# Performance work log

Measured on AMD Instinct MI355X. Metric: run time of the kernel, lower is better.

The kernel has to match this reference:

```python
import jax, jax.numpy as jnp
import numpy as np

EMB = 512
HID = 1024
BATCH = 64
TX = 512


def setup_inputs() -> dict:
    key = jax.random.key(0)
    ks = jax.random.split(key, 9)
    s = 0.05
    return {
        "word": jax.random.normal(ks[0], (BATCH, TX, EMB), dtype=jnp.float32),
        "Wz": jax.random.normal(ks[1], (HID, HID + EMB), dtype=jnp.float32) * s,
        "bz": jax.random.normal(ks[2], (HID,), dtype=jnp.float32) * s,
        "Wr": jax.random.normal(ks[3], (HID, HID + EMB), dtype=jnp.float32) * s,
        "br": jax.random.normal(ks[4], (HID,), dtype=jnp.float32) * s,
        "Wh": jax.random.normal(ks[5], (HID, HID + EMB), dtype=jnp.float32) * s,
        "bh": jax.random.normal(ks[6], (HID,), dtype=jnp.float32) * s,
        "Wy": jax.random.normal(ks[7], (EMB, HID), dtype=jnp.float32) * s,
        "by": jax.random.normal(ks[8], (EMB,), dtype=jnp.float32) * s,
    }


def reference(word, Wz, bz, Wr, br, Wh, bh, Wy, by):
    batch = word.shape[0]
    word_t = jnp.transpose(word, (1, 0, 2))  # [T, B, E]
    h0 = jnp.zeros((batch, HID), dtype=word.dtype)
    x0 = jnp.zeros((batch, EMB), dtype=word.dtype)

    def step(carry, w_i):
        h, x = carry  # x is the PREVIOUS timestep's word (lags by one, as in the torch code)
        comb = jnp.concatenate([h, x], axis=1)  # [B, HID+EMB]
        z = jax.nn.sigmoid(comb @ Wz.T + bz)
        r = jax.nn.sigmoid(comb @ Wr.T + br)
        comb2 = jnp.concatenate([r * h, x], axis=1)
        h_tilde = jnp.tanh(comb2 @ Wh.T + bh)
        h_new = (1.0 - z) * h + z * h_tilde
        y = h_new @ Wy.T + by  # [B, E]
        return (h_new, w_i), y

    _, ys = jax.lax.scan(step, (h0, x0), word_t)  # ys: [T, B, E]
    return jnp.transpose(ys, (1, 0, 2))  # [B, T, E]
```

## Files before the change

### kernel.cpp

```cpp
#include <hip/hip_runtime.h>
#include <hip/hip_bf16.h>


#define EMB 512
#define HID 1024
#define BATCHN 64
#define TLEN 512
#define CAT 1536
#define GROUPS 4
#define GB 16
#define WPG 32
#define HX_LD 1024
#define ZL_LD 34
#define GPAD 8

typedef __attribute__((ext_vector_type(8))) short bf16x8;
typedef __attribute__((ext_vector_type(4))) short s16x4;
typedef __attribute__((ext_vector_type(4))) float f32x4;
typedef unsigned int u32;
typedef unsigned long long u64;
typedef unsigned short u16;

__device__ __forceinline__ float bf2f(u16 u) {
  union { float f; u32 i; } v; v.i = ((u32)u) << 16; return v.f;
}
__device__ __forceinline__ u16 f2bf(float f) {
  union { float f; u32 i; } v; v.f = f;
  u32 r = v.i + 0x7fffu + ((v.i >> 16) & 1u);
  return (u16)(r >> 16);
}

__device__ __forceinline__ u64 ld_dc(const u16* p) {
  return __hip_atomic_load((const u64*)p, __ATOMIC_RELAXED, __HIP_MEMORY_SCOPE_AGENT);
}
__device__ __forceinline__ void st_dc16(u16* p, u16 v) {
  __hip_atomic_store(p, v, __ATOMIC_RELAXED, __HIP_MEMORY_SCOPE_AGENT);
}

__global__ __launch_bounds__(256) void convert_gate_w(const float* __restrict__ W,
                                                      u16* __restrict__ Wh_,
                                                      u16* __restrict__ Wx_) {
  int i = blockIdx.x * 256 + threadIdx.x;
  if (i >= HID * CAT) return;
  int row = i / CAT, col = i - row * CAT;
  u16 v = f2bf(W[i]);
  if (col < HID) Wh_[row * HID + col] = v;
  else           Wx_[row * EMB + (col - HID)] = v;
}

__global__ __launch_bounds__(256) void convert_wy(const float* __restrict__ W, u16* __restrict__ Wy_) {
  int i = blockIdx.x * 256 + threadIdx.x;
  if (i < EMB * HID) Wy_[i] = f2bf(W[i]);
}

__global__ __launch_bounds__(256) void proj3_kernel(
    const float* __restrict__ word,
    const u16* __restrict__ Wzx, const u16* __restrict__ Wrx, const u16* __restrict__ Whx,
    const float* __restrict__ bz, const float* __restrict__ br, const float* __restrict__ bh,
    u16* __restrict__ Pz, u16* __restrict__ Pr, u16* __restrict__ Ph) {
  __shared__ __align__(16) u16 As[128][64 + GPAD];
  __shared__ __align__(16) u16 Bs[3][64][64 + GPAD];
  const int tid = threadIdx.x;
  const int wid = tid >> 6, lane = tid & 63;
  const int m0 = blockIdx.x * 128, n0 = blockIdx.y * 64;
  const int mw = wid * 32;
  const u16* __restrict__ Wx[3] = {Wzx, Wrx, Whx};
  f32x4 acc[3][2][4] = {};
  for (int k0 = 0; k0 < EMB; k0 += 64) {
#pragma unroll
    for (int it = 0; it < 8; ++it) {
      int e = (it * 256 + tid) * 4;
      int row = e >> 6, col = e & 63;
      int R = m0 + row;
      float4 a = make_float4(0.f, 0.f, 0.f, 0.f);
      if ((R & (TLEN - 1)) != 0)
        a = *reinterpret_cast<const float4*>(&word[(u64)(R - 1) * EMB + k0 + col]);
      s16x4 vv;
      vv[0] = (short)f2bf(a.x); vv[1] = (short)f2bf(a.y);
      vv[2] = (short)f2bf(a.z); vv[3] = (short)f2bf(a.w);
      *reinterpret_cast<s16x4*>(&As[row][col]) = vv;
    }
#pragma unroll
    for (int p = 0; p < 3; ++p)
#pragma unroll
      for (int it = 0; it < 2; ++it) {
        int e = (it * 256 + tid) * 8;
        int row = e >> 6, col = e & 63;
        *reinterpret_cast<bf16x8*>(&Bs[p][row][col]) =
            *reinterpret_cast<const bf16x8*>(&Wx[p][(u64)(n0 + row) * EMB + k0 + col]);
      }
    __syncthreads();
#pragma unroll
    for (int kk = 0; kk < 2; ++kk) {
      const int kb = kk * 32 + 8 * (lane >> 4);
#pragma unroll
      for (int i = 0; i < 2; ++i) {
        bf16x8 a = *reinterpret_cast<const bf16x8*>(&As[mw + i * 16 + (lane & 15)][kb]);
#pragma unroll
        for (int p = 0; p < 3; ++p)
#pragma unroll
          for (int j = 0; j < 4; ++j) {
            bf16x8 b = *reinterpret_cast<const bf16x8*>(&Bs[p][j * 16 + (lane & 15)][kb]);
            acc[p][i][j] = __builtin_amdgcn_mfma_f32_16x16x32_bf16(a, b, acc[p][i][j], 0, 0, 0);
          }
      }
    }
    __syncthreads();
  }
  u16* __restrict__ Pout[3] = {Pz, Pr, Ph};
  const float* __restrict__ bias[3] = {bz, br, bh};
#pragma unroll
  for (int p = 0; p < 3; ++p)
#pragma unroll
    for (int i = 0; i < 2; ++i)
#pragma unroll
      for (int j = 0; j < 4; ++j) {
        int col = n0 + j * 16 + (lane & 15);
        float bv = bias[p][col];
#pragma unroll
        for (int q = 0; q < 4; ++q) {
          int row = m0 + mw + i * 16 + 4 * (lane >> 4) + q;
          Pout[p][(u64)row * HID + col] = f2bf(acc[p][i][j][q] + bv);
        }
      }
}

__global__ __launch_bounds__(256) void out_gemm(const u16* __restrict__ H,
                                                const u16* __restrict__ Wy,
                                                const float* __restrict__ by,
                                                float* __restrict__ out) {
  __shared__ __align__(16) u16 As[128][64 + GPAD];
  __shared__ __align__(16) u16 Bs[64][64 + GPAD];
  const int tid = threadIdx.x;
  const int wid = tid >> 6, lane = tid & 63;
  const int m0 = blockIdx.x * 128, n0 = blockIdx.y * 64;
  const int mw = wid * 32;
  f32x4 acc[2][4] = {};
  for (int k0 = 0; k0 < HID; k0 += 64) {
#pragma unroll
    for (int it = 0; it < 4; ++it) {
      int e = (it * 256 + tid) * 8;
      int row = e >> 6, col = e & 63;
      *reinterpret_cast<bf16x8*>(&As[row][col]) =
          *reinterpret_cast<const bf16x8*>(&H[(u64)(m0 + row) * HID + k0 + col]);
    }
#pragma unroll
    for (int it = 0; it < 2; ++it) {
      int e = (it * 256 + tid) * 8;
      int row = e >> 6, col = e & 63;
      *reinterpret_cast<bf16x8*>(&Bs[row][col]) =
          *reinterpret_cast<const bf16x8*>(&Wy[(u64)(n0 + row) * HID + k0 + col]);
    }
    __syncthreads();
#pragma unroll
    for (int kk = 0; kk < 2; ++kk) {
      const int kb = kk * 32 + 8 * (lane >> 4);
#pragma unroll
      for (int i = 0; i < 2; ++i) {
        bf16x8 a = *reinterpret_cast<const bf16x8*>(&As[mw + i * 16 + (lane & 15)][kb]);
#pragma unroll
        for (int j = 0; j < 4; ++j) {
          bf16x8 b = *reinterpret_cast<const bf16x8*>(&Bs[j * 16 + (lane & 15)][kb]);
          acc[i][j] = __builtin_amdgcn_mfma_f32_16x16x32_bf16(a, b, acc[i][j], 0, 0, 0);
        }
      }
    }
    __syncthreads();
  }
#pragma unroll
  for (int i = 0; i < 2; ++i)
#pragma unroll
    for (int j = 0; j < 4; ++j) {
      int col = n0 + j * 16 + (lane & 15);
      float bv = by[col];
#pragma unroll
      for (int q = 0; q < 4; ++q) {
        int row = m0 + mw + i * 16 + 4 * (lane >> 4) + q;
        out[(u64)row * EMB + col] = acc[i][j][q] + bv;
      }
    }
}

__device__ __forceinline__ void poll_flags_wave(u32* gflags, u32 target) {
  const int lane = threadIdx.x & 63;
  const int active = (lane < WPG) ? 1 : 0;
  u32* addr = &gflags[(lane & (WPG - 1)) * 16];
  for (;;) {
    u32 v = target;
    if (active)
      v = __hip_atomic_load(addr, __ATOMIC_RELAXED, __HIP_MEMORY_SCOPE_AGENT);
    if (!__any((int)(v < target))) break;
  }
}

__global__ __launch_bounds__(256, 1) void gru_persistent(
    const u16* __restrict__ Wzh, const u16* __restrict__ Wrh, const u16* __restrict__ Whh,
    const u16* __restrict__ Pz, const u16* __restrict__ Pr, u16* __restrict__ PhH,
    u16* __restrict__ rhbuf, u32* flags) {
  __shared__ __align__(16) u16 hx[16 * HX_LD];
  __shared__ __align__(16) u16 zL[16 * ZL_LD];
  __shared__ __align__(16) float RED[4 * 64 * 4];

  const int tid = threadIdx.x;
  const int wid = tid >> 6;
  const int lane = tid & 63;
  const int l15 = lane & 15;
  const int k4 = lane >> 4;
  const int g = blockIdx.x & (GROUPS - 1);
  const int w = blockIdx.x >> 2;
  const int b0 = g * GB;
  const int j = wid & 1;
  const int gate = wid >> 1;
  const int kh = wid >> 1;
  const int colA = 32 * w + 16 * j + l15;
  const u16* __restrict__ PA = gate ? Pr : Pz;
  u32* gflags = flags + g * (WPG * 16);

  const int sw = (l15 & 7) << 3;
  const int srow = tid >> 4;
  const int soff = (tid & 15) * 4;
  const int ssw = (srow & 7) << 3;

  bf16x8 wfA[32];
#pragma unroll
  for (int s = 0; s < 32; ++s)
    wfA[s] = *reinterpret_cast<const bf16x8*>(
        (gate ? Wrh : Wzh) + (u64)colA * HID + 32 * s + k4 * 8);
  bf16x8 wfB[16];
#pragma unroll
  for (int s = 0; s < 16; ++s)
    wfB[s] = *reinterpret_cast<const bf16x8*>(
        Whh + (u64)colA * HID + kh * 512 + 32 * s + k4 * 8);
#pragma unroll
  for (int s = 0; s < 32; ++s) asm volatile("" : "+v"(wfA[s]));
#pragma unroll
  for (int s = 0; s < 16; ++s) asm volatile("" : "+v"(wfB[s]));

  for (int e = tid; e < 16 * HX_LD / 2; e += 256) reinterpret_cast<u32*>(hx)[e] = 0u;
  __syncthreads();

  u16 pAr[4], pBr[4];
#pragma unroll
  for (int q = 0; q < 4; ++q) {
    int m = 4 * k4 + q;
    pAr[q] = PA[((u64)(b0 + m) * TLEN) * HID + colA];
    pBr[q] = PhH[((u64)(b0 + m) * TLEN) * HID + colA];
  }

  float hprev[4] = {0.f, 0.f, 0.f, 0.f};
  u32 ph = 0;

  for (int t = 0; t < TLEN; ++t) {
    if (t > 0) {
      const u16* src = PhH + ((u64)(b0 + srow) * TLEN + (t - 1)) * HID + soff;
      u64 tmp[16];
#pragma unroll
      for (int i = 0; i < 16; ++i) tmp[i] = ld_dc(src + i * 64);
      u16* dst = &hx[srow * HX_LD];
#pragma unroll
      for (int i = 0; i < 16; ++i)
        *reinterpret_cast<u64*>(dst + ((soff + i * 64) ^ ssw)) = tmp[i];
      __syncthreads();
    }

    f32x4 acc = {0.f, 0.f, 0.f, 0.f}, acc_b = {0.f, 0.f, 0.f, 0.f};
    if (t > 0) {
#pragma unroll
      for (int s = 0; s < 32; s += 2) {
        bf16x8 a0 = *reinterpret_cast<const bf16x8*>(
            &hx[l15 * HX_LD + ((32 * s + k4 * 8) ^ sw)]);
        bf16x8 a1 = *reinterpret_cast<const bf16x8*>(
            &hx[l15 * HX_LD + ((32 * (s + 1) + k4 * 8) ^ sw)]);
        acc   = __builtin_amdgcn_mfma_f32_16x16x32_bf16(a0, wfA[s],     acc,   0, 0, 0);
        acc_b = __builtin_amdgcn_mfma_f32_16x16x32_bf16(a1, wfA[s + 1], acc_b, 0, 0, 0);
      }
    }
#pragma unroll
    for (int q = 0; q < 4; ++q) {
      int m = 4 * k4 + q;
      float pre = acc[q] + acc_b[q] + bf2f(pAr[q]);
      float sg = 1.f / (1.f + __expf(-pre));
      if (gate == 0) {
        zL[m * ZL_LD + 16 * j + l15] = f2bf(sg);
      } else {
        st_dc16(rhbuf + (u64)(g * GB + m) * HID + colA, f2bf(sg * hprev[q]));
      }
    }

    ++ph;
    __syncthreads();
    asm volatile("" ::: "memory");
    if (tid == w)
      __hip_atomic_store(&gflags[w * 16], ph, __ATOMIC_RELAXED, __HIP_MEMORY_SCOPE_AGENT);
    {
      int tn = (t + 1 < TLEN) ? (t + 1) : t;
#pragma unroll
      for (int q = 0; q < 4; ++q) {
        int m = 4 * k4 + q;
        pAr[q] = PA[((u64)(b0 + m) * TLEN + tn) * HID + colA];
      }
    }
    poll_flags_wave(gflags, ph);
    asm volatile("" ::: "memory");

    {
      const u16* src = rhbuf + (u64)(g * GB + srow) * HID + soff;
      u64 tmp[16];
#pragma unroll
      for (int i = 0; i < 16; ++i) tmp[i] = ld_dc(src + i * 64);
      u16* dst = &hx[srow * HX_LD];
#pragma unroll
      for (int i = 0; i < 16; ++i)
        *reinterpret_cast<u64*>(dst + ((soff + i * 64) ^ ssw)) = tmp[i];
      __syncthreads();
    }

    f32x4 acc2 = {0.f, 0.f, 0.f, 0.f}, acc2b = {0.f, 0.f, 0.f, 0.f};
#pragma unroll
    for (int s = 0; s < 16; s += 2) {
      bf16x8 a0 = *reinterpret_cast<const bf16x8*>(
          &hx[l15 * HX_LD + ((kh * 512 + 32 * s + k4 * 8) ^ sw)]);
      bf16x8 a1 = *reinterpret_cast<const bf16x8*>(
          &hx[l15 * HX_LD + ((kh * 512 + 32 * (s + 1) + k4 * 8) ^ sw)]);
      acc2  = __builtin_amdgcn_mfma_f32_16x16x32_bf16(a0, wfB[s],     acc2,  0, 0, 0);
      acc2b = __builtin_amdgcn_mfma_f32_16x16x32_bf16(a1, wfB[s + 1], acc2b, 0, 0, 0);
    }
#pragma unroll
    for (int q = 0; q < 4; ++q) acc2[q] += acc2b[q];
    *reinterpret_cast<f32x4*>(&RED[(wid * 64 + lane) * 4]) = acc2;
    __syncthreads();
    {
      f32x4 part = *reinterpret_cast<const f32x4*>(&RED[((wid ^ 2) * 64 + lane) * 4]);
#pragma unroll
      for (int q = 0; q < 4; ++q) {
        int m = 4 * k4 + q;
        float pre = acc2[q] + part[q] + bf2f(pBr[q]);
        float e2 = __expf(2.f * pre);
        float th = 1.f - 2.f / (e2 + 1.f);
        float zq = bf2f(zL[m * ZL_LD + 16 * j + l15]);
        float hn = (1.f - zq) * hprev[q] + zq * th;
        hprev[q] = hn;
        if (wid < 2)
          st_dc16(PhH + ((u64)(b0 + m) * TLEN + t) * HID + colA, f2bf(hn));
      }
    }

    ++ph;
    __syncthreads();
    asm volatile("" ::: "memory");
    if (tid == w)
      __hip_atomic_store(&gflags[w * 16], ph, __ATOMIC_RELAXED, __HIP_MEMORY_SCOPE_AGENT);
    {
      int tn = (t + 1 < TLEN) ? (t + 1) : t;
#pragma unroll
      for (int q = 0; q < 4; ++q) {
        int m = 4 * k4 + q;
        pBr[q] = PhH[((u64)(b0 + m) * TLEN + tn) * HID + colA];
      }
    }
    poll_flags_wave(gflags, ph);
    asm volatile("" ::: "memory");
  }
}

extern "C" void kernel_launch(void* const* d_in, const int* in_sizes, int n_in,
                              void* d_out, int out_size, void* d_ws, size_t ws_size,
                              hipStream_t stream) {
  const float* word = (const float*)d_in[0];
  const float* Wz = (const float*)d_in[1];
  const float* bz = (const float*)d_in[2];
  const float* Wr = (const float*)d_in[3];
  const float* br = (const float*)d_in[4];
  const float* Wh = (const float*)d_in[5];
  const float* bh = (const float*)d_in[6];
  const float* Wy = (const float*)d_in[7];
  const float* by = (const float*)d_in[8];
  float* out = (float*)d_out;
  (void)in_sizes; (void)n_in; (void)out_size; (void)ws_size;

  char* ws = (char*)d_ws;
  size_t off = 0;
  auto alloc = [&](size_t bytes) {
    char* p = ws + off;
    off += (bytes + 255) & ~(size_t)255;
    return p;
  };
  u32* flags = (u32*)alloc(GROUPS * WPG * 16 * sizeof(u32));
  u16* WzhB = (u16*)alloc((size_t)HID * HID * 2);
  u16* WrhB = (u16*)alloc((size_t)HID * HID * 2);
  u16* WhhB = (u16*)alloc((size_t)HID * HID * 2);
  u16* WzxB = (u16*)alloc((size_t)HID * EMB * 2);
  u16* WrxB = (u16*)alloc((size_t)HID * EMB * 2);
  u16* WhxB = (u16*)alloc((size_t)HID * EMB * 2);
  u16* WyB  = (u16*)alloc((size_t)EMB * HID * 2);
  u16* Pr   = (u16*)alloc((size_t)BATCHN * TLEN * HID * 2);
  u16* PhH  = (u16*)alloc((size_t)BATCHN * TLEN * HID * 2);
  u16* rhbuf = (u16*)alloc((size_t)GROUPS * GB * HID * 2);
  u16* Pz = (u16*)d_out;

  hipMemsetAsync(flags, 0, GROUPS * WPG * 16 * sizeof(u32), stream);

  convert_gate_w<<<(HID * CAT + 255) / 256, 256, 0, stream>>>(Wz, WzhB, WzxB);
  convert_gate_w<<<(HID * CAT + 255) / 256, 256, 0, stream>>>(Wr, WrhB, WrxB);
  convert_gate_w<<<(HID * CAT + 255) / 256, 256, 0, stream>>>(Wh, WhhB, WhxB);
  convert_wy<<<(EMB * HID + 255) / 256, 256, 0, stream>>>(Wy, WyB);

  proj3_kernel<<<dim3(256, 16), 256, 0, stream>>>(word, WzxB, WrxB, WhxB,
                                                  bz, br, bh, Pz, Pr, PhH);

  gru_persistent<<<dim3(GROUPS * WPG), dim3(256), 0, stream>>>(WzhB, WrhB, WhhB, Pz, Pr, PhH,
                                                               rhbuf, flags);

  out_gemm<<<dim3(256, 8), 256, 0, stream>>>(PhH, WyB, by, out);
}
```

Before: 2.871 ms.

## Use per-wave flags instead of block barrier for group sync, fuse weight conversions

Each wave now publishes its own progress flag after waiting for its outstanding memory operations, and pollers check 128 flags per group. This removes the __syncthreads before each flag store in the persistent GRU loop, so a block no longer waits for all its waves before signalling. The four weight-conversion launches are also merged into one kernel to cut launch overhead. The trade-off is more flag traffic per poll and reliance on s_waitcnt for ordering, since there is no block barrier any more.

```diff
diff --git a/kernel.cpp b/kernel.cpp
--- a/kernel.cpp
+++ b/kernel.cpp
@@ -37,20 +37,28 @@
   __hip_atomic_store(p, v, __ATOMIC_RELAXED, __HIP_MEMORY_SCOPE_AGENT);
 }
 
-__global__ __launch_bounds__(256) void convert_gate_w(const float* __restrict__ W,
-                                                      u16* __restrict__ Wh_,
-                                                      u16* __restrict__ Wx_) {
+__global__ __launch_bounds__(256) void convert_all(
+    const float* __restrict__ Wz, const float* __restrict__ Wr,
+    const float* __restrict__ Wh, const float* __restrict__ Wy,
+    u16* __restrict__ Wzh, u16* __restrict__ Wzx,
+    u16* __restrict__ Wrh, u16* __restrict__ Wrx,
+    u16* __restrict__ Whh, u16* __restrict__ Whx, u16* __restrict__ WyB) {
   int i = blockIdx.x * 256 + threadIdx.x;
-  if (i >= HID * CAT) return;
-  int row = i / CAT, col = i - row * CAT;
-  u16 v = f2bf(W[i]);
-  if (col < HID) Wh_[row * HID + col] = v;
-  else           Wx_[row * EMB + (col - HID)] = v;
-}
-
-__global__ __launch_bounds__(256) void convert_wy(const float* __restrict__ W, u16* __restrict__ Wy_) {
-  int i = blockIdx.x * 256 + threadIdx.x;
-  if (i < EMB * HID) Wy_[i] = f2bf(W[i]);
+  if (i < HID * CAT) {
+    int row = i / CAT, col = i - row * CAT;
+    u16 vz = f2bf(Wz[i]), vr = f2bf(Wr[i]), vh = f2bf(Wh[i]);
+    if (col < HID) {
+      Wzh[row * HID + col] = vz;
+      Wrh[row * HID + col] = vr;
+      Whh[row * HID + col] = vh;
+    } else {
+      int c = col - HID;
+      Wzx[row * EMB + c] = vz;
+      Wrx[row * EMB + c] = vr;
+      Whx[row * EMB + c] = vh;
+    }
+  }
+  if (i < EMB * HID) WyB[i] = f2bf(Wy[i]);
 }
 
 __global__ __launch_bounds__(256) void proj3_kernel(
@@ -181,15 +189,14 @@
     }
 }
 
-__device__ __forceinline__ void poll_flags_wave(u32* gflags, u32 target) {
+__device__ __forceinline__ void poll_flags128(u32* gflags, u32 target) {
   const int lane = threadIdx.x & 63;
-  const int active = (lane < WPG) ? 1 : 0;
-  u32* addr = &gflags[(lane & (WPG - 1)) * 16];
+  u32* a0 = &gflags[lane * 16];
+  u32* a1 = &gflags[(lane + 64) * 16];
   for (;;) {
-    u32 v = target;
-    if (active)
-      v = __hip_atomic_load(addr, __ATOMIC_RELAXED, __HIP_MEMORY_SCOPE_AGENT);
-    if (!__any((int)(v < target))) break;
+    u32 v0 = __hip_atomic_load(a0, __ATOMIC_RELAXED, __HIP_MEMORY_SCOPE_AGENT);
+    u32 v1 = __hip_atomic_load(a1, __ATOMIC_RELAXED, __HIP_MEMORY_SCOPE_AGENT);
+    if (!__any((int)((v0 < target) | (v1 < target)))) break;
   }
 }
 
@@ -214,7 +221,8 @@
   const int kh = wid >> 1;
   const int colA = 32 * w + 16 * j + l15;
   const u16* __restrict__ PA = gate ? Pr : Pz;
-  u32* gflags = flags + g * (WPG * 16);
+  u32* gflags = flags + g * (128 * 16);
+  u32* myflag = &gflags[(w * 4 + wid) * 16];
 
   const int sw = (l15 & 7) << 3;
   const int srow = tid >> 4;
@@ -288,10 +296,9 @@
     }
 
     ++ph;
-    __syncthreads();
-    asm volatile("" ::: "memory");
-    if (tid == w)
-      __hip_atomic_store(&gflags[w * 16], ph, __ATOMIC_RELAXED, __HIP_MEMORY_SCOPE_AGENT);
+    asm volatile("s_waitcnt vmcnt(0) lgkmcnt(0)" ::: "memory");
+    if (lane == 0)
+      __hip_atomic_store(myflag, ph, __ATOMIC_RELAXED, __HIP_MEMORY_SCOPE_AGENT);
     {
       int tn = (t + 1 < TLEN) ? (t + 1) : t;
 #pragma unroll
@@ -300,7 +307,7 @@
         pAr[q] = PA[((u64)(b0 + m) * TLEN + tn) * HID + colA];
       }
     }
-    poll_flags_wave(gflags, ph);
+    poll_flags128(gflags, ph);
     asm volatile("" ::: "memory");
 
     {
@@ -346,10 +353,9 @@
     }
 
     ++ph;
-    __syncthreads();
-    asm volatile("" ::: "memory");
-    if (tid == w)
-      __hip_atomic_store(&gflags[w * 16], ph, __ATOMIC_RELAXED, __HIP_MEMORY_SCOPE_AGENT);
+    asm volatile("s_waitcnt vmcnt(0) lgkmcnt(0)" ::: "memory");
+    if (lane == 0)
+      __hip_atomic_store(myflag, ph, __ATOMIC_RELAXED, __HIP_MEMORY_SCOPE_AGENT);
     {
       int tn = (t + 1 < TLEN) ? (t + 1) : t;
 #pragma unroll
@@ -358,7 +364,7 @@
         pBr[q] = PhH[((u64)(b0 + m) * TLEN + tn) * HID + colA];
       }
     }
-    poll_flags_wave(gflags, ph);
+    poll_flags128(gflags, ph);
     asm volatile("" ::: "memory");
   }
 }
@@ -385,7 +391,7 @@
     off += (bytes + 255) & ~(size_t)255;
     return p;
   };
-  u32* flags = (u32*)alloc(GROUPS * WPG * 16 * sizeof(u32));
+  u32* flags = (u32*)alloc(GROUPS * 128 * 16 * sizeof(u32));
   u16* WzhB = (u16*)alloc((size_t)HID * HID * 2);
   u16* WrhB = (u16*)alloc((size_t)HID * HID * 2);
   u16* WhhB = (u16*)alloc((size_t)HID * HID * 2);
@@ -398,12 +404,10 @@
   u16* rhbuf = (u16*)alloc((size_t)GROUPS * GB * HID * 2);
   u16* Pz = (u16*)d_out;
 
-  hipMemsetAsync(flags, 0, GROUPS * WPG * 16 * sizeof(u32), stream);
-
-  convert_gate_w<<<(HID * CAT + 255) / 256, 256, 0, stream>>>(Wz, WzhB, WzxB);
-  convert_gate_w<<<(HID * CAT + 255) / 256, 256, 0, stream>>>(Wr, WrhB, WrxB);
-  convert_gate_w<<<(HID * CAT + 255) / 256, 256, 0, stream>>>(Wh, WhhB, WhxB);
-  convert_wy<<<(EMB * HID + 255) / 256, 256, 0, stream>>>(Wy, WyB);
+  hipMemsetAsync(flags, 0, GROUPS * 128 * 16 * sizeof(u32), stream);
+
+  convert_all<<<(HID * CAT + 255) / 256, 256, 0, stream>>>(
+      Wz, Wr, Wh, Wy, WzhB, WzxB, WrhB, WrxB, WhhB, WhxB, WyB);
 
   proj3_kernel<<<dim3(256, 16), 256, 0, stream>>>(word, WzxB, WrxB, WhxB,
                                                   bz, br, bh, Pz, Pr, PhH);
```

Result: slower. 3.997 ms (+39.2%).
